# Kernel tuning notes

Hardware: AMD Instinct MI355X
Metric: run time of the kernel (lower is better)

The kernel has to match this reference:

```python
import jax, jax.numpy as jnp
import numpy as np

COMMITMENT_COST = 0.25


def setup_inputs() -> dict:
    key = jax.random.key(0)
    k1, k2 = jax.random.split(key)
    x = jax.random.normal(k1, (32, 256, 32, 32), dtype=jnp.float32)          # NCHW latents
    embedding = jax.random.normal(k2, (1024, 256), dtype=jnp.float32)        # [K, D] codebook
    return {"x": x, "embedding": embedding}


def reference(x, embedding):
    # NCHW -> NHWC, flatten to [N, D]
    inp = jnp.transpose(x, (0, 2, 3, 1))
    B, H, W, D = inp.shape
    K = embedding.shape[0]
    flat = inp.reshape(-1, D)                                                # [N, D]

    dists = (jnp.sum(flat * flat, axis=1, keepdims=True)
             + jnp.sum(embedding * embedding, axis=1)
             - 2.0 * flat @ embedding.T)
    idx = jnp.argmin(dists, axis=1)                                          # [N]
    encodings = jax.nn.one_hot(idx, K, dtype=flat.dtype)                     # [N, K]

    quantized = (encodings @ embedding).reshape(B, H, W, D)

    # commitment loss (codebook detached, eval path: no EMA update)
    e_latent_loss = jnp.mean(jnp.square(jax.lax.stop_gradient(quantized) - inp))
    loss = COMMITMENT_COST * e_latent_loss

    # straight-through estimator
    quantized_st = inp + jax.lax.stop_gradient(quantized - inp)

    avg_probs = jnp.mean(encodings, axis=0)
    perplexity = jnp.exp(-jnp.sum(avg_probs * jnp.log(avg_probs + 1e-10)))

    return (loss, jnp.transpose(quantized_st, (0, 3, 1, 2)), perplexity, encodings)
```

## Files before the change

kernel.cpp:

```cpp
#include <hip/hip_runtime.h>
#include <math.h>

#define D    256
#define K    1024
#define HWX  1024
#define NPTS 32768
#define PT   64
#define NPAIR 32

#define Q_OFF    1
#define PERP_OFF (1 + 8388608)
#define ENC_OFF  (2 + 8388608)

#define WS_FRAG_OFF 16384

typedef __attribute__((ext_vector_type(8))) short bf16x8;
typedef __attribute__((ext_vector_type(4))) float f32x4;

__device__ __forceinline__ unsigned short bf16_rne(float f) {
  unsigned int u = __float_as_uint(f);
  u = u + 0x7fffu + ((u >> 16) & 1u);
  return (unsigned short)(u >> 16);
}

#define CONV(F, H, L)                                                          \
  {                                                                            \
    H = bf16_rne(F);                                                           \
    const float fh_ = __uint_as_float((unsigned)(H) << 16);                    \
    L = bf16_rne((F)-fh_);                                                     \
  }

__global__ __launch_bounds__(256) void vq_frag(const float* __restrict__ emb,
                                               unsigned int* __restrict__ frag,
                                               float* __restrict__ enorm,
                                               int* __restrict__ counts,
                                               float* __restrict__ loss_accum) {
  const int gid = blockIdx.x * 256 + threadIdx.x;
  const int c = gid >> 5, g = gid & 31;
  const float* src = emb + (size_t)c * D + g * 8;
  const float4 a = *(const float4*)src;
  const float4 b = *(const float4*)(src + 4);
  float s = a.x * a.x + a.y * a.y + a.z * a.z + a.w * a.w +
            b.x * b.x + b.y * b.y + b.z * b.z + b.w * b.w;
#pragma unroll
  for (int off = 1; off < 32; off <<= 1) s += __shfl_xor(s, off);
  if (g == 0) enorm[c] = s;
  unsigned short h0, h1, h2, h3, h4, h5, h6, h7;
  unsigned short l0, l1, l2, l3, l4, l5, l6, l7;
  CONV(a.x, h0, l0) CONV(a.y, h1, l1) CONV(a.z, h2, l2) CONV(a.w, h3, l3)
  CONV(b.x, h4, l4) CONV(b.y, h5, l5) CONV(b.z, h6, l6) CONV(b.w, h7, l7)
  uint4 uh, ul;
  uh.x = (unsigned)h0 | ((unsigned)h1 << 16); uh.y = (unsigned)h2 | ((unsigned)h3 << 16);
  uh.z = (unsigned)h4 | ((unsigned)h5 << 16); uh.w = (unsigned)h6 | ((unsigned)h7 << 16);
  ul.x = (unsigned)l0 | ((unsigned)l1 << 16); ul.y = (unsigned)l2 | ((unsigned)l3 << 16);
  ul.z = (unsigned)l4 | ((unsigned)l5 << 16); ul.w = (unsigned)l6 | ((unsigned)l7 << 16);
  const int fragidx = (c >> 4) * 16 + (g >> 2) * 2;
  const int Lo = ((c & 15) + 16 * (g & 3)) * 4;
  *(uint4*)(frag + (size_t)fragidx * 256 + Lo) = uh;
  *(uint4*)(frag + (size_t)(fragidx + 1) * 256 + Lo) = ul;
  if (gid < K) counts[gid] = 0;
  if (gid == 0) *loss_accum = 0.0f;
}

#define ISSUE_PAIR(P, SEL)                                                     \
  {                                                                            \
    const unsigned* gsrc = fragg + (((size_t)(P)*32 + w * 8) * 256) + lane * 4; \
    unsigned short* ldst = fbuf + (SEL)*16384 + (w * 8) * 512;                 \
    _Pragma("unroll") for (int q = 0; q < 8; ++q)                              \
        __builtin_amdgcn_global_load_lds(                                      \
            (const __attribute__((address_space(1))) unsigned*)(gsrc + q * 256), \
            (__attribute__((address_space(3))) unsigned*)(ldst + q * 512),     \
            16, 0, 0);                                                         \
  }

#define AH(RTL, KS)                                                            \
  ah##RTL##_##KS = *(const bf16x8*)&fbuf[(((pg * 2 + RTL) * 8 + KS) * 2 + 0) * 512 + lane * 8]; \
  al##RTL##_##KS = *(const bf16x8*)&fbuf[(((pg * 2 + RTL) * 8 + KS) * 2 + 1) * 512 + lane * 8];

#define KS(KSv)                                                                \
  {                                                                            \
    const bf16x8 bh = *(const bf16x8*)&fbuf[bufo + (KSv * 2 + 0) * 512 + lane * 8]; \
    const bf16x8 bl = *(const bf16x8*)&fbuf[bufo + (KSv * 2 + 1) * 512 + lane * 8]; \
    acc0 = __builtin_amdgcn_mfma_f32_16x16x32_bf16(ah0_##KSv, bh, acc0, 0, 0, 0); \
    acc0 = __builtin_amdgcn_mfma_f32_16x16x32_bf16(al0_##KSv, bh, acc0, 0, 0, 0); \
    acc0 = __builtin_amdgcn_mfma_f32_16x16x32_bf16(ah0_##KSv, bl, acc0, 0, 0, 0); \
    acc0 = __builtin_amdgcn_mfma_f32_16x16x32_bf16(al0_##KSv, bl, acc0, 0, 0, 0); \
    acc1 = __builtin_amdgcn_mfma_f32_16x16x32_bf16(ah1_##KSv, bh, acc1, 0, 0, 0); \
    acc1 = __builtin_amdgcn_mfma_f32_16x16x32_bf16(al1_##KSv, bh, acc1, 0, 0, 0); \
    acc1 = __builtin_amdgcn_mfma_f32_16x16x32_bf16(ah1_##KSv, bl, acc1, 0, 0, 0); \
    acc1 = __builtin_amdgcn_mfma_f32_16x16x32_bf16(al1_##KSv, bl, acc1, 0, 0, 0); \
  }

__global__ __launch_bounds__(256) void vq_main(const float* __restrict__ x,
                                               const unsigned int* __restrict__ fragg,
                                               const float* __restrict__ emb,
                                               const float* __restrict__ enorm,
                                               float* __restrict__ out_q,
                                               float* __restrict__ out_enc,
                                               float* __restrict__ loss_accum,
                                               int* __restrict__ counts) {
  __shared__ __align__(16) unsigned short fbuf[32768];
  __shared__ float en_s[K];
  __shared__ float xn_part[256];
  __shared__ float red_val[128];
  __shared__ int red_idx[128];
  __shared__ int idx_s[PT];

  const int t = threadIdx.x;
  const int lane = t & 63;
  const int w = t >> 6;
  const int pg = w >> 1;
  const int par = w & 1;
  const int p0 = blockIdx.x * PT;
  const int bb = p0 >> 10;
  const int hw0 = p0 & 1023;

  {
    const int pt = t & 63, c0 = t >> 6;
    const int rt = pt >> 4, mrow = pt & 15;
    const float* xb = x + (size_t)bb * (D * HWX) + hw0 + pt;
    float xn = 0.0f;
    for (int c = c0; c < D; c += 4) {
      const float f = xb[(size_t)c * HWX];
      unsigned short h, l;
      CONV(f, h, l)
      xn += f * f;
      const int ks = c >> 5, quad = (c >> 3) & 3, j = c & 7;
      const int Lr = mrow + 16 * quad;
      fbuf[((rt * 8 + ks) * 2 + 0) * 512 + Lr * 8 + j] = h;
      fbuf[((rt * 8 + ks) * 2 + 1) * 512 + Lr * 8 + j] = l;
    }
    xn_part[t] = xn;
  }
  for (int i = t; i < K; i += 256) en_s[i] = enorm[i];
  __syncthreads();

  bf16x8 ah0_0, ah0_1, ah0_2, ah0_3, ah0_4, ah0_5, ah0_6, ah0_7;
  bf16x8 al0_0, al0_1, al0_2, al0_3, al0_4, al0_5, al0_6, al0_7;
  bf16x8 ah1_0, ah1_1, ah1_2, ah1_3, ah1_4, ah1_5, ah1_6, ah1_7;
  bf16x8 al1_0, al1_1, al1_2, al1_3, al1_4, al1_5, al1_6, al1_7;
  AH(0, 0) AH(0, 1) AH(0, 2) AH(0, 3) AH(0, 4) AH(0, 5) AH(0, 6) AH(0, 7)
  AH(1, 0) AH(1, 1) AH(1, 2) AH(1, 3) AH(1, 4) AH(1, 5) AH(1, 6) AH(1, 7)
  __syncthreads();

  float mv[8];
  int mi[8];
#pragma unroll
  for (int i = 0; i < 8; ++i) { mv[i] = 3.4e38f; mi[i] = 0; }

  ISSUE_PAIR(0, 0)
  int sel = 0;
  for (int p = 0; p < NPAIR; ++p) {
    __syncthreads();
    if (p + 1 < NPAIR) ISSUE_PAIR(p + 1, sel ^ 1)
    const int bufo = sel * 16384 + par * 16 * 512;
    f32x4 acc0 = {0.f, 0.f, 0.f, 0.f};
    f32x4 acc1 = {0.f, 0.f, 0.f, 0.f};
    KS(0) KS(1) KS(2) KS(3) KS(4) KS(5) KS(6) KS(7)
    const int code = (p * 2 + par) * 16 + (lane & 15);
    const float en_l = en_s[code];
    float m;
    m = en_l - 2.0f * acc0[0]; if (m < mv[0]) { mv[0] = m; mi[0] = code; }
    m = en_l - 2.0f * acc0[1]; if (m < mv[1]) { mv[1] = m; mi[1] = code; }
    m = en_l - 2.0f * acc0[2]; if (m < mv[2]) { mv[2] = m; mi[2] = code; }
    m = en_l - 2.0f * acc0[3]; if (m < mv[3]) { mv[3] = m; mi[3] = code; }
    m = en_l - 2.0f * acc1[0]; if (m < mv[4]) { mv[4] = m; mi[4] = code; }
    m = en_l - 2.0f * acc1[1]; if (m < mv[5]) { mv[5] = m; mi[5] = code; }
    m = en_l - 2.0f * acc1[2]; if (m < mv[6]) { mv[6] = m; mi[6] = code; }
    m = en_l - 2.0f * acc1[3]; if (m < mv[7]) { mv[7] = m; mi[7] = code; }
    sel ^= 1;
  }

#pragma unroll
  for (int off = 1; off < 16; off <<= 1) {
#pragma unroll
    for (int i = 0; i < 8; ++i) {
      const float ov = __shfl_xor(mv[i], off);
      const int oi = __shfl_xor(mi[i], off);
      if (ov < mv[i] || (ov == mv[i] && oi < mi[i])) { mv[i] = ov; mi[i] = oi; }
    }
  }
  if ((lane & 15) == 0) {
    const int quad = lane >> 4;
#pragma unroll
    for (int i = 0; i < 8; ++i) {
      const int loc = (i >> 2) * 16 + quad * 4 + (i & 3);
      red_val[w * 32 + loc] = mv[i];
      red_idx[w * 32 + loc] = mi[i];
    }
  }
  __syncthreads();
  float dist = 0.0f;
  if (t < PT) {
    const int pgm = t >> 5, loc = t & 31;
    float bv = red_val[(pgm * 2) * 32 + loc];
    int bi = red_idx[(pgm * 2) * 32 + loc];
    const float v1 = red_val[(pgm * 2 + 1) * 32 + loc];
    const int i1 = red_idx[(pgm * 2 + 1) * 32 + loc];
    if (v1 < bv || (v1 == bv && i1 < bi)) { bv = v1; bi = i1; }
    float xn = 0.0f;
#pragma unroll
    for (int g = 0; g < 4; ++g) xn += xn_part[t + 64 * g];
    dist = bv + xn;
    idx_s[t] = bi;
    atomicAdd(&counts[bi], 1);
  }
  if (t < 64) {
#pragma unroll
    for (int off = 32; off > 0; off >>= 1) dist += __shfl_down(dist, off);
    if (t == 0) atomicAdd(loss_accum, dist);
  }
  __syncthreads();

  {
    const int pt = t & 63, c0 = t >> 6;
    const int row = idx_s[pt];
    const float* er = emb + (size_t)row * D;
    float* qb = out_q + (size_t)bb * D * HWX + hw0 + pt;
#pragma unroll
    for (int c = c0; c < D; c += 4) qb[(size_t)c * HWX] = er[c];
  }
  {
    float2* eb2 = reinterpret_cast<float2*>(out_enc + (size_t)p0 * K);
#pragma unroll 4
    for (int i = t; i < PT * K / 2; i += 256) {
      const int row = i >> 9;
      const int c2 = (i & 511) * 2;
      const int target = idx_s[row];
      float2 v = make_float2(0.f, 0.f);
      if (target == c2) v.x = 1.0f;
      else if (target == c2 + 1) v.y = 1.0f;
      eb2[i] = v;
    }
  }
}

__global__ __launch_bounds__(256) void vq_final(const int* __restrict__ counts,
                                                const float* __restrict__ loss_accum,
                                                float* __restrict__ out) {
  __shared__ float sh[4];
  const int t = threadIdx.x;
  float s = 0.0f;
  for (int k = t; k < K; k += 256) {
    const float p = (float)counts[k] * (1.0f / 32768.0f);
    s += p * logf(p + 1e-10f);
  }
#pragma unroll
  for (int off = 32; off > 0; off >>= 1) s += __shfl_down(s, off);
  if ((t & 63) == 0) sh[t >> 6] = s;
  __syncthreads();
  if (t == 0) {
    const float tot = sh[0] + sh[1] + sh[2] + sh[3];
    out[PERP_OFF] = expf(-tot);
    out[0] = 0.25f * (*loss_accum) / 8388608.0f;
  }
}

extern "C" void kernel_launch(void* const* d_in, const int* in_sizes, int n_in,
                              void* d_out, int out_size, void* d_ws, size_t ws_size,
                              hipStream_t stream) {
  const float* x = (const float*)d_in[0];
  const float* emb = (const float*)d_in[1];
  float* out = (float*)d_out;
  float* enorm = (float*)d_ws;
  int* counts = (int*)((char*)d_ws + 4096);
  float* loss_accum = (float*)((char*)d_ws + 8192);
  unsigned int* fragg = (unsigned int*)((char*)d_ws + WS_FRAG_OFF);

  hipLaunchKernelGGL(vq_frag, dim3(128), dim3(256), 0, stream,
                     emb, fragg, enorm, counts, loss_accum);
  hipLaunchKernelGGL(vq_main, dim3(NPTS / PT), dim3(256), 0, stream,
                     x, fragg, emb, enorm, out + Q_OFF, out + ENC_OFF,
                     loss_accum, counts);
  hipLaunchKernelGGL(vq_final, dim3(1), dim3(256), 0, stream,
                     counts, loss_accum, out);
}
```

Before: 287.7 us.

## Split VQ epilogue into separate kernel with LDS-staged coalesced codebook gather

Moves the quantized-output gather and one-hot encoding writes out of the GEMM/argmin kernel into a new epilogue kernel, passing indices through a workspace buffer. The epilogue loads codebook rows with float4 reads into padded shared memory, then writes NCHW output, replacing strided per-channel scalar reads. This frees the GEMM kernel from the large store tail so its occupancy and latency are not tied to output writes, and lets the store-bound epilogue run with more, smaller blocks. It costs an extra kernel launch and a small global round-trip for indices.

```diff
diff --git a/kernel.cpp b/kernel.cpp
--- a/kernel.cpp
+++ b/kernel.cpp
@@ -12,7 +12,8 @@
 #define PERP_OFF (1 + 8388608)
 #define ENC_OFF  (2 + 8388608)
 
-#define WS_FRAG_OFF 16384
+#define WS_IDX_OFF  16384
+#define WS_FRAG_OFF 147456
 
 typedef __attribute__((ext_vector_type(8))) short bf16x8;
 typedef __attribute__((ext_vector_type(4))) float f32x4;
@@ -91,12 +92,10 @@
     acc1 = __builtin_amdgcn_mfma_f32_16x16x32_bf16(al1_##KSv, bl, acc1, 0, 0, 0); \
   }
 
-__global__ __launch_bounds__(256) void vq_main(const float* __restrict__ x,
+__global__ __launch_bounds__(256) void vq_gemm(const float* __restrict__ x,
                                                const unsigned int* __restrict__ fragg,
-                                               const float* __restrict__ emb,
                                                const float* __restrict__ enorm,
-                                               float* __restrict__ out_q,
-                                               float* __restrict__ out_enc,
+                                               int* __restrict__ idxb,
                                                float* __restrict__ loss_accum,
                                                int* __restrict__ counts) {
   __shared__ __align__(16) unsigned short fbuf[32768];
@@ -104,7 +103,6 @@
   __shared__ float xn_part[256];
   __shared__ float red_val[128];
   __shared__ int red_idx[128];
-  __shared__ int idx_s[PT];
 
   const int t = threadIdx.x;
   const int lane = t & 63;
@@ -202,7 +200,7 @@
 #pragma unroll
     for (int g = 0; g < 4; ++g) xn += xn_part[t + 64 * g];
     dist = bv + xn;
-    idx_s[t] = bi;
+    idxb[p0 + t] = bi;
     atomicAdd(&counts[bi], 1);
   }
   if (t < 64) {
@@ -210,20 +208,44 @@
     for (int off = 32; off > 0; off >>= 1) dist += __shfl_down(dist, off);
     if (t == 0) atomicAdd(loss_accum, dist);
   }
+}
+
+__global__ __launch_bounds__(256) void vq_epi(const int* __restrict__ idxb,
+                                              const float* __restrict__ emb,
+                                              float* __restrict__ out_q,
+                                              float* __restrict__ out_enc) {
+  __shared__ float xq[32 * 257];
+  __shared__ int idx_s[32];
+  const int t = threadIdx.x;
+  const int lane = t & 63;
+  const int w = t >> 6;
+  const int p0 = blockIdx.x * 32;
+  const int bb = p0 >> 10;
+  const int hw0 = p0 & 1023;
+
+  if (t < 32) idx_s[t] = idxb[p0 + t];
+  __syncthreads();
+
+  for (int r = w; r < 32; r += 4) {
+    const float4 v = ((const float4*)(emb + (size_t)idx_s[r] * D))[lane];
+    float* dst = &xq[r * 257 + lane];
+    dst[0] = v.x; dst[64] = v.y; dst[128] = v.z; dst[192] = v.w;
+  }
   __syncthreads();
 
   {
-    const int pt = t & 63, c0 = t >> 6;
-    const int row = idx_s[pt];
-    const float* er = emb + (size_t)row * D;
+    const int pt = t & 31, c0 = t >> 5;
     float* qb = out_q + (size_t)bb * D * HWX + hw0 + pt;
 #pragma unroll
-    for (int c = c0; c < D; c += 4) qb[(size_t)c * HWX] = er[c];
+    for (int ci = c0; ci < D; ci += 8) {
+      const int pos = (ci >> 2) + 64 * (ci & 3);
+      qb[(size_t)ci * HWX] = xq[pt * 257 + pos];
+    }
   }
   {
     float2* eb2 = reinterpret_cast<float2*>(out_enc + (size_t)p0 * K);
 #pragma unroll 4
-    for (int i = t; i < PT * K / 2; i += 256) {
+    for (int i = t; i < 32 * K / 2; i += 256) {
       const int row = i >> 9;
       const int c2 = (i & 511) * 2;
       const int target = idx_s[row];
@@ -265,13 +287,15 @@
   float* enorm = (float*)d_ws;
   int* counts = (int*)((char*)d_ws + 4096);
   float* loss_accum = (float*)((char*)d_ws + 8192);
+  int* idxb = (int*)((char*)d_ws + WS_IDX_OFF);
   unsigned int* fragg = (unsigned int*)((char*)d_ws + WS_FRAG_OFF);
 
   hipLaunchKernelGGL(vq_frag, dim3(128), dim3(256), 0, stream,
                      emb, fragg, enorm, counts, loss_accum);
-  hipLaunchKernelGGL(vq_main, dim3(NPTS / PT), dim3(256), 0, stream,
-                     x, fragg, emb, enorm, out + Q_OFF, out + ENC_OFF,
-                     loss_accum, counts);
+  hipLaunchKernelGGL(vq_gemm, dim3(NPTS / PT), dim3(256), 0, stream,
+                     x, fragg, enorm, idxb, loss_accum, counts);
+  hipLaunchKernelGGL(vq_epi, dim3(NPTS / 32), dim3(256), 0, stream,
+                     idxb, emb, out + Q_OFF, out + ENC_OFF);
   hipLaunchKernelGGL(vq_final, dim3(1), dim3(256), 0, stream,
                      counts, loss_accum, out);
 }
```

New measurement: 299.5 us. 1.04x slower.
